# Performance work log

Hardware: AMD Instinct MI355X
Metric: run time of the kernel (lower is better)

Reference implementation:

```python
import jax, jax.numpy as jnp
import numpy as np

MODES1 = 20
MODES2 = 20
WIDTH = 64
NUM_LAYERS = 4
B, H, W = 8, 256, 256


def _conv2d(x, w, b, pad):
    # x: (B,C,H,W), w: (O,I,kh,kw)
    y = jax.lax.conv_general_dilated(
        x, w, window_strides=(1, 1), padding=[(pad, pad), (pad, pad)],
        dimension_numbers=('NCHW', 'OIHW', 'NCHW'))
    return y + b[None, :, None, None]


def _spectral_conv(x, w1, w2, m1, m2):
    # x: (B,C,H,W); w1,w2: (I,O,m1,m2,2) real/imag pairs
    h, w = x.shape[-2], x.shape[-1]
    x_ft = jnp.fft.rfft2(x, norm='ortho')              # (B,C,H,W//2+1) complex
    w1c = w1[..., 0] + 1j * w1[..., 1]
    w2c = w2[..., 0] + 1j * w2[..., 1]
    top = jnp.einsum('bixy,ioxy->boxy', x_ft[:, :, :m1, :m2], w1c)
    bot = jnp.einsum('bixy,ioxy->boxy', x_ft[:, :, -m1:, :m2], w2c)
    out_ft = jnp.zeros((x.shape[0], w1.shape[1], h, w // 2 + 1), dtype=x_ft.dtype)
    out_ft = out_ft.at[:, :, :m1, :m2].set(top)
    out_ft = out_ft.at[:, :, -m1:, :m2].set(bot)
    return jnp.fft.irfft2(out_ft, s=(h, w), norm='ortho')


def setup_inputs() -> dict:
    key = jax.random.key(0)
    ks = jax.random.split(key, 16)
    C = WIDTH
    L = NUM_LAYERS
    scale = 1.0 / (C * C)
    inp = {
        'x': jax.random.normal(ks[0], (B, H, W, 3), dtype=jnp.float32),
        'fc0_w': jax.random.normal(ks[1], (3, C), dtype=jnp.float32) * 0.1,
        'fc0_b': jnp.zeros((C,), dtype=jnp.float32),
        'w1': scale * jax.random.uniform(ks[2], (L, C, C, MODES1, MODES2, 2), dtype=jnp.float32),
        'w2': scale * jax.random.uniform(ks[3], (L, C, C, MODES1, MODES2, 2), dtype=jnp.float32),
        'convh_w': jax.random.normal(ks[4], (L, C, C, 3, 3), dtype=jnp.float32) * 0.02,
        'convh_b': jnp.zeros((L, C), dtype=jnp.float32),
        'convw_w': jax.random.normal(ks[5], (L, C, C, 3, 3), dtype=jnp.float32) * 0.02,
        'convw_b': jnp.zeros((L, C), dtype=jnp.float32),
        'pw_w': jax.random.normal(ks[6], (L, C, C, 1, 1), dtype=jnp.float32) * 0.05,
        'pw_b': jnp.zeros((L, C), dtype=jnp.float32),
        'fc1_w': jax.random.normal(ks[7], (C, 128), dtype=jnp.float32) * 0.05,
        'fc1_b': jnp.zeros((128,), dtype=jnp.float32),
        'fc2_w': jax.random.normal(ks[8], (128, 1), dtype=jnp.float32) * 0.05,
        'fc2_b': jnp.zeros((1,), dtype=jnp.float32),
    }
    return inp


def reference(x, fc0_w, fc0_b, w1, w2, convh_w, convh_b, convw_w, convw_b,
              pw_w, pw_b, fc1_w, fc1_b, fc2_w, fc2_b):
    # fc0 lift: (B,H,W,3) -> (B,H,W,C) -> (B,C,H,W)
    h = jnp.einsum('bhwc,cd->bhwd', x, fc0_w) + fc0_b
    h = jnp.transpose(h, (0, 3, 1, 2))
    for i in range(NUM_LAYERS):
        x1 = _spectral_conv(h, w1[i], w2[i], MODES1, MODES2)
        # Mamba fallback block: two 3x3 convs summed (LayerNorm unused in forward)
        x2 = _conv2d(h, convh_w[i], convh_b[i], 1) + _conv2d(h, convw_w[i], convw_b[i], 1)
        x3 = _conv2d(h, pw_w[i], pw_b[i], 0)
        h = x1 + x2 + x3
        if i < NUM_LAYERS - 1:
            h = jax.nn.gelu(h, approximate=False)
    h = jnp.transpose(h, (0, 2, 3, 1))                  # (B,H,W,C)
    h = jnp.einsum('bhwc,cd->bhwd', h, fc1_w) + fc1_b
    h = jax.nn.gelu(h, approximate=False)
    out = jnp.einsum('bhwc,cd->bhwd', h, fc2_w) + fc2_b  # (B,H,W,1)
    return out
```

## Files before the change

### kernel.cpp

```cpp
#include <hip/hip_runtime.h>
#include <math.h>

#define NB 8
#define NC 64
#define NH 256
#define NW 256
#define NM 40
#define NKX 20
#define NL 4

typedef _Float16 f16x8 __attribute__((ext_vector_type(8)));
typedef float    f32x4 __attribute__((ext_vector_type(4)));

#define PERCB_FLOATS ((size_t)(2*4194304 + 655360 + 2*102400))
#define FIXED_FLOATS ((size_t)(6553600 + 10240 + 20480 + 147456 + 256 + 167936 + 2048))

static __device__ __forceinline__ float gelu_f(float v) {
  return 0.5f * v * (1.f + erff(v * 0.70710678118654752f));
}
static __device__ __forceinline__ unsigned pack2(_Float16 a, _Float16 b) {
  union { _Float16 h[2]; unsigned u; } x; x.h[0] = a; x.h[1] = b; return x.u;
}

__global__ __launch_bounds__(256) void k_tables(float2* __restrict__ Tx,
                                                float2* __restrict__ Ty) {
  int t = blockIdx.x * 256 + threadIdx.x;
  const float w = (float)(2.0 * 3.14159265358979323846 / 256.0);
  if (t < NKX * 256) {
    int kx = t >> 8, x = t & 255;
    float th = (float)((kx * x) & 255) * w;
    Tx[t] = make_float2(cosf(th), sinf(th));
  }
  int u = t - NKX * 256;
  if (u >= 0 && u < NM * 256) {
    int m = u >> 8, y = u & 255;
    int ky = (m < 20) ? m : (m + 216);
    float th = (float)((ky * y) & 255) * w;
    Ty[u] = make_float2(cosf(th), sinf(th));
  }
}

__global__ __launch_bounds__(256) void k_txpack(_Float16* __restrict__ th,
                                                _Float16* __restrict__ tl) {
  int t = blockIdx.x * 256 + threadIdx.x;
  int j = t & 7, lane = (t >> 3) & 63;
  int rest = t >> 9;
  int nt = rest % 3, kc = rest / 3;
  int x = kc * 32 + ((lane >> 4) << 3) + j;
  int n = nt * 16 + (lane & 15);
  float val = 0.f;
  if (n < 40) {
    int kx = n >> 1;
    const float w = (float)(2.0 * 3.14159265358979323846 / 256.0);
    float ang = (float)((kx * x) & 255) * w;
    val = (n & 1) ? -sinf(ang) : cosf(ang);
  }
  _Float16 hi = (_Float16)val;
  th[t] = hi;
  tl[t] = (_Float16)(val - (float)hi);
}

__global__ __launch_bounds__(256) void k_wc(const float* __restrict__ ch,
                                            const float* __restrict__ cw,
                                            const float* __restrict__ pw,
                                            const float* __restrict__ chb,
                                            const float* __restrict__ cwb,
                                            const float* __restrict__ pwb,
                                            float* __restrict__ wc,
                                            float* __restrict__ bc) {
  int t = blockIdx.x * 256 + threadIdx.x;
  if (t < NL * NC * NC * 9) {
    int tap = t % 9;
    int io  = t / 9;
    int o   = io % 64;
    int i   = (io / 64) % 64;
    int l   = io / 4096;
    int src = ((l * 64 + o) * 64 + i) * 9 + tap;
    float v = ch[src] + cw[src];
    if (tap == 4) v += pw[(l * 64 + o) * 64 + i];
    wc[t] = v;
  }
  if (t < NL * NC) bc[t] = chb[t] + cwb[t] + pwb[t];
}

__global__ __launch_bounds__(256) void k_wpack(const float* __restrict__ wc,
                                               _Float16* __restrict__ whi,
                                               _Float16* __restrict__ wlo) {
  int t = blockIdx.x * 256 + threadIdx.x;
  int lane = t & 63;
  int nt   = (t >> 6) & 3;
  int chunk = (t >> 8) % 18;
  int l4   = t / 4608;
  int tap = chunk >> 1, half = chunk & 1;
  int o = nt * 16 + (lane & 15);
  _Float16 hi[8], lo[8];
  #pragma unroll
  for (int j = 0; j < 8; ++j) {
    int i = half * 32 + ((lane >> 4) << 3) + j;
    float v = wc[((l4 * 64 + i) * 64 + o) * 9 + tap];
    _Float16 h = (_Float16)v;
    hi[j] = h;
    lo[j] = (_Float16)(v - (float)h);
  }
  *(f16x8*)(whi + (size_t)t * 8) = *(f16x8*)hi;
  *(f16x8*)(wlo + (size_t)t * 8) = *(f16x8*)lo;
}

__global__ __launch_bounds__(256) void k_hpack(const float* __restrict__ w1,
                                               _Float16* __restrict__ whi,
                                               _Float16* __restrict__ wlo) {
  int t = blockIdx.x * 256 + threadIdx.x;
  int lane = t & 63;
  int nt   = (t >> 6) & 7;
  int chunk = t >> 9;
  int jo = nt * 16 + (lane & 15);
  _Float16 hi[8], lo[8];
  #pragma unroll
  for (int j = 0; j < 8; ++j) {
    int c = chunk * 32 + ((lane >> 4) << 3) + j;
    float v = w1[c * 128 + jo];
    _Float16 h = (_Float16)v;
    hi[j] = h;
    lo[j] = (_Float16)(v - (float)h);
  }
  *(f16x8*)(whi + (size_t)t * 8) = *(f16x8*)hi;
  *(f16x8*)(wlo + (size_t)t * 8) = *(f16x8*)lo;
}

__global__ __launch_bounds__(256) void k_fc0(const float* __restrict__ x,
                                             const float* __restrict__ w,
                                             const float* __restrict__ b,
                                             float* __restrict__ h, int b0) {
  int t = blockIdx.x * 256 + threadIdx.x;
  int ch = t & 63;
  int px = t >> 6;
  const float* xp = x + ((size_t)b0 * 65536 + px) * 3;
  h[t] = xp[0] * w[ch] + xp[1] * w[64 + ch] + xp[2] * w[128 + ch] + b[ch];
}

__global__ __launch_bounds__(256) void k_fwdx(const float* __restrict__ h,
                                              const f16x8* __restrict__ txh,
                                              const f16x8* __restrict__ txl,
                                              float2* __restrict__ Fx) {
  __shared__ _Float16 sH[64 * 136 * 2];
  int y = blockIdx.x & 255, bb = blockIdx.x >> 8;
  int tid = threadIdx.x;
  int w = tid >> 6, lane = tid & 63, quad = lane >> 4, l15 = lane & 15;
  const float* hp = h + ((size_t)(bb * 256 + y) * 256) * 64;

  f32x4 acc[3];
  #pragma unroll
  for (int nt = 0; nt < 3; ++nt) acc[nt] = (f32x4){0.f, 0.f, 0.f, 0.f};

  #pragma unroll 1
  for (int hs = 0; hs < 2; ++hs) {
    __syncthreads();
    #pragma unroll
    for (int it = 0; it < 8; ++it) {
      int e = it * 256 + tid;
      int xx = e >> 4;
      int chg = (e & 15) << 2;
      float4 v = *(const float4*)(hp + ((size_t)(hs * 128 + xx)) * 64 + chg);
      float vv[4] = {v.x, v.y, v.z, v.w};
      #pragma unroll
      for (int k = 0; k < 4; ++k) {
        _Float16 hi = (_Float16)vv[k];
        sH[(chg + k) * 136 + xx] = hi;
        sH[8704 + (chg + k) * 136 + xx] = (_Float16)(vv[k] - (float)hi);
      }
    }
    __syncthreads();
    #pragma unroll
    for (int kc = 0; kc < 4; ++kc) {
      int xb = kc * 32 + (quad << 3);
      f16x8 ah = *(const f16x8*)(sH + (w * 16 + l15) * 136 + xb);
      f16x8 al = *(const f16x8*)(sH + 8704 + (w * 16 + l15) * 136 + xb);
      int kcg = hs * 4 + kc;
      #pragma unroll
      for (int nt = 0; nt < 3; ++nt) {
        f16x8 bh = txh[(size_t)(kcg * 3 + nt) * 64 + lane];
        f16x8 bl = txl[(size_t)(kcg * 3 + nt) * 64 + lane];
        acc[nt] = __builtin_amdgcn_mfma_f32_16x16x32_f16(ah, bh, acc[nt], 0, 0, 0);
        acc[nt] = __builtin_amdgcn_mfma_f32_16x16x32_f16(ah, bl, acc[nt], 0, 0, 0);
        acc[nt] = __builtin_amdgcn_mfma_f32_16x16x32_f16(al, bh, acc[nt], 0, 0, 0);
      }
    }
  }
  #pragma unroll
  for (int nt = 0; nt < 3; ++nt) {
    int n = nt * 16 + l15;
    if (n < 40) {
      int kx = n >> 1, ri = n & 1;
      #pragma unroll
      for (int r = 0; r < 4; ++r) {
        int c = w * 16 + (quad << 2) + r;
        ((float*)(Fx + ((size_t)(bb * 64 + c) * 256 + y) * 20 + kx))[ri] = acc[nt][r];
      }
    }
  }
}

__global__ __launch_bounds__(256) void k_fwdy(const float2* __restrict__ Fx,
                                              const float2* __restrict__ Ty,
                                              float2* __restrict__ FxyT, int nbc) {
  __shared__ float2 sFx[5120];
  int bc = blockIdx.x;
  const float4* src = (const float4*)(Fx + (size_t)bc * 5120);
  float4* dst = (float4*)sFx;
  for (int e = threadIdx.x; e < 2560; e += 256) dst[e] = src[e];
  __syncthreads();
  for (int mk = threadIdx.x; mk < 800; mk += 256) {
    int kx = mk % 20, m = mk / 20;
    const float2* tp = Ty + m * 256;
    float re = 0.f, im = 0.f;
    #pragma unroll 4
    for (int yy = 0; yy < 256; ++yy) {
      float2 f = sFx[yy * 20 + kx];
      float2 wv = tp[yy];
      re += f.x * wv.x + f.y * wv.y;
      im += f.y * wv.x - f.x * wv.y;
    }
    FxyT[(size_t)mk * nbc + bc] = make_float2(re * (1.f / 256.f), im * (1.f / 256.f));
  }
}

__global__ __launch_bounds__(256) void k_wT(const float* __restrict__ w1,
                                            const float* __restrict__ w2,
                                            float2* __restrict__ wT, int l) {
  __shared__ float2 tile[32][33];
  int mk0 = blockIdx.x * 32;
  int io0 = blockIdx.y * 32;
  int tx = threadIdx.x & 31, ty0 = threadIdx.x >> 5;
  #pragma unroll
  for (int s = 0; s < 4; ++s) {
    int ty = ty0 * 4 + s;
    int mk = mk0 + tx, io = io0 + ty;
    int m = mk / 20, kx = mk % 20;
    const float* src = (m < 20) ? w1 : w2;
    int mm = (m < 20) ? m : (m - 20);
    size_t idx = ((((size_t)l * 4096 + io) * 20 + mm) * 20 + kx) * 2;
    tile[ty][tx] = make_float2(src[idx], src[idx + 1]);
  }
  __syncthreads();
  #pragma unroll
  for (int s = 0; s < 4; ++s) {
    int ty = ty0 * 4 + s;
    wT[(size_t)(mk0 + ty) * 4096 + (io0 + tx)] = tile[tx][ty];
  }
}

__global__ __launch_bounds__(256) void k_mix(const float2* __restrict__ FxyT,
                                             const float2* __restrict__ wT,
                                             float2* __restrict__ G, int nrows) {
  __shared__ float2 sf[512];
  int mk = blockIdx.x;
  for (int t = threadIdx.x; t < nrows; t += 256)
    sf[t] = FxyT[(size_t)mk * nrows + t];
  __syncthreads();
  const float2* wp = wT + (size_t)mk * 4096;
  for (int t = threadIdx.x; t < nrows; t += 256) {
    int b = t >> 6, o = t & 63;
    const float2* fb = sf + b * 64;
    float re = 0.f, im = 0.f;
    #pragma unroll 8
    for (int i = 0; i < 64; ++i) {
      float2 f = fb[i];
      float2 w = wp[i * 64 + o];
      re += f.x * w.x - f.y * w.y;
      im += f.x * w.y + f.y * w.x;
    }
    G[(size_t)(b * 64 + o) * 800 + mk] = make_float2(re, im);
  }
}

__global__ __launch_bounds__(256) void k_invy(const float2* __restrict__ G,
                                              const float2* __restrict__ Ty,
                                              float2* __restrict__ Gy) {
  int t  = blockIdx.x * 256 + threadIdx.x;
  int kx = t % 20;
  int y  = (t / 20) & 255;
  int bc = t / 5120;
  const float2* gp = G + (size_t)bc * 800 + kx;
  float re = 0.f, im = 0.f;
  #pragma unroll 4
  for (int m = 0; m < 40; ++m) {
    float2 g = gp[m * 20];
    float2 w = Ty[m * 256 + y];
    re += g.x * w.x - g.y * w.y;
    im += g.x * w.y + g.y * w.x;
  }
  Gy[t] = make_float2(re, im);
}

__global__ __launch_bounds__(256, 3) void k_conv(const float* __restrict__ hin,
                                                 const f16x8* __restrict__ wph,
                                                 const f16x8* __restrict__ wpl,
                                                 const float* __restrict__ bcb,
                                                 const float2* __restrict__ Gy,
                                                 const float2* __restrict__ Tx,
                                                 float* __restrict__ hout,
                                                 int dogelu, int bsh) {
  __shared__ unsigned sAu[13056];
  int bidx = blockIdx.x;
  int bb = bidx & ((1 << bsh) - 1);
  int rest = bidx >> bsh;
  int xt = rest & 7;
  int yt = (rest >> 3) & 63;
  int x0 = xt << 5, y0 = yt << 2;
  int tid = threadIdx.x;
  int w = tid >> 6, lane = tid & 63, quad = lane >> 4, l15 = lane & 15;

  float bias[4];
  #pragma unroll
  for (int nt = 0; nt < 4; ++nt) bias[nt] = bcb[nt * 16 + l15];

  for (int e = tid; e < 204 * 32; e += 256) {
    int px = e >> 5, chp = e & 31;
    int rg = px / 34, cg = px % 34;
    int gy = y0 - 1 + rg, gx = x0 - 1 + cg;
    float2 v = make_float2(0.f, 0.f);
    if (gy >= 0 && gy < 256 && gx >= 0 && gx < 256)
      v = *(const float2*)(hin + (((size_t)bb * 256 + gy) * 256 + gx) * 64 + chp * 2);
    _Float16 h0 = (_Float16)v.x, h1 = (_Float16)v.y;
    _Float16 l0 = (_Float16)(v.x - (float)h0), l1 = (_Float16)(v.y - (float)h1);
    int dw = (px << 5) + (chp ^ ((px & 7) << 2));
    sAu[dw] = pack2(h0, h1);
    sAu[6528 + dw] = pack2(l0, l1);
  }
  __syncthreads();

  f32x4 acc[2][4];
  #pragma unroll
  for (int s = 0; s < 2; ++s)
    #pragma unroll
    for (int nt = 0; nt < 4; ++nt) acc[s][nt] = (f32x4){0.f, 0.f, 0.f, 0.f};

  #pragma unroll 1
  for (int tap = 0; tap < 9; ++tap) {
    int dy = tap / 3, dx = tap % 3;
    #pragma unroll
    for (int half = 0; half < 2; ++half) {
      int chunk = tap * 2 + half;
      const f16x8* bh = wph + (size_t)(chunk * 4) * 64 + lane;
      const f16x8* bl = wpl + (size_t)(chunk * 4) * 64 + lane;
      f16x8 bfh[4], bfl[4];
      #pragma unroll
      for (int nt = 0; nt < 4; ++nt) { bfh[nt] = bh[nt * 64]; bfl[nt] = bl[nt * 64]; }
      f16x8 afh[2], afl[2];
      #pragma unroll
      for (int s = 0; s < 2; ++s) {
        int px = (w + dy) * 34 + (s * 16 + dx) + l15;
        int dw = (px << 5) + (((half << 4) + (quad << 2)) ^ ((px & 7) << 2));
        afh[s] = *(const f16x8*)(sAu + dw);
        afl[s] = *(const f16x8*)(sAu + 6528 + dw);
      }
      #pragma unroll
      for (int s = 0; s < 2; ++s)
        #pragma unroll
        for (int nt = 0; nt < 4; ++nt) {
          acc[s][nt] = __builtin_amdgcn_mfma_f32_16x16x32_f16(afh[s], bfh[nt], acc[s][nt], 0, 0, 0);
          acc[s][nt] = __builtin_amdgcn_mfma_f32_16x16x32_f16(afh[s], bfl[nt], acc[s][nt], 0, 0, 0);
          acc[s][nt] = __builtin_amdgcn_mfma_f32_16x16x32_f16(afl[s], bfh[nt], acc[s][nt], 0, 0, 0);
        }
    }
  }

  __syncthreads();
  float2* sT  = (float2*)sAu;
  float2* sGy = (float2*)(sAu + 1280);
  for (int e = tid; e < 640; e += 256) {
    int kx = e >> 5, col = e & 31;
    sT[e] = Tx[kx * 256 + x0 + col];
  }
  for (int e = tid; e < 5120; e += 256) {
    int o = e / 80, rem = e % 80;
    int row = rem / 20, kx = rem % 20;
    sGy[o * 82 + row * 20 + kx] =
        Gy[((size_t)(bb * 64 + o) * 256 + (y0 + row)) * 20 + kx];
  }
  __syncthreads();

  const float scale = 1.f / 256.f;
  #pragma unroll
  for (int s = 0; s < 2; ++s) {
    int colb = s * 16 + (quad << 2);
    #pragma unroll
    for (int nt = 0; nt < 4; ++nt) {
      int o = nt * 16 + l15;
      const float2* gp = sGy + o * 82 + w * 20;
      f32x4 sr = {0.f, 0.f, 0.f, 0.f};
      #pragma unroll
      for (int p = 0; p < 10; ++p) {
        float4 g = *(const float4*)(gp + 2 * p);
        float f0 = (p == 0) ? 1.f : 2.f;
        float4 tA = *(const float4*)(sT + (2 * p) * 32 + colb);
        float4 tB = *(const float4*)(sT + (2 * p) * 32 + colb + 2);
        sr.x += f0 * (g.x * tA.x - g.y * tA.y);
        sr.y += f0 * (g.x * tA.z - g.y * tA.w);
        sr.z += f0 * (g.x * tB.x - g.y * tB.y);
        sr.w += f0 * (g.x * tB.z - g.y * tB.w);
        float4 tC = *(const float4*)(sT + (2 * p + 1) * 32 + colb);
        float4 tD = *(const float4*)(sT + (2 * p + 1) * 32 + colb + 2);
        sr.x += 2.f * (g.z * tC.x - g.w * tC.y);
        sr.y += 2.f * (g.z * tC.z - g.w * tC.w);
        sr.z += 2.f * (g.z * tD.x - g.w * tD.y);
        sr.w += 2.f * (g.z * tD.z - g.w * tD.w);
      }
      #pragma unroll
      for (int r = 0; r < 4; ++r) {
        float v = acc[s][nt][r] + bias[nt] + sr[r] * scale;
        if (dogelu) v = gelu_f(v);
        acc[s][nt][r] = v;
      }
    }
  }

  __syncthreads();
  float* sF = (float*)sAu;
  #pragma unroll
  for (int s = 0; s < 2; ++s)
    #pragma unroll
    for (int nt = 0; nt < 4; ++nt)
      #pragma unroll
      for (int r = 0; r < 4; ++r) {
        int c = s * 16 + (quad << 2) + r;
        int seg = nt ^ ((c >> 2) & 3);
        sF[(w * 32 + c) * 64 + seg * 16 + l15] = acc[s][nt][r];
      }
  __syncthreads();

  float* op = hout + (((size_t)bb * 256 + (y0 + w)) * 256 + x0) * 64;
  #pragma unroll
  for (int i = 0; i < 8; ++i) {
    int chunk = i * 64 + lane;
    int c = chunk >> 4, ch4 = chunk & 15;
    int seg = (ch4 >> 2) ^ ((c >> 2) & 3);
    float4 v = *(const float4*)(sF + (w * 32 + c) * 64 + seg * 16 + (ch4 & 3) * 4);
    *(float4*)(op + c * 64 + ch4 * 4) = v;
  }
}

__global__ __launch_bounds__(256, 2) void k_head(const float* __restrict__ h,
                                                 const f16x8* __restrict__ whi,
                                                 const f16x8* __restrict__ wlo,
                                                 const float* __restrict__ b1,
                                                 const float* __restrict__ w2,
                                                 const float* __restrict__ b2,
                                                 float* __restrict__ out, int b0) {
  int tid = threadIdx.x;
  int w = tid >> 6, lane = tid & 63, quad = lane >> 4, l15 = lane & 15;
  int px0 = blockIdx.x * 64 + w * 16;

  f32x4 acc[8];
  #pragma unroll
  for (int nt = 0; nt < 8; ++nt) acc[nt] = (f32x4){0.f, 0.f, 0.f, 0.f};

  #pragma unroll
  for (int half = 0; half < 2; ++half) {
    const float* ap = h + (size_t)(px0 + l15) * 64 + half * 32 + quad * 8;
    float4 a0 = *(const float4*)ap;
    float4 a1 = *(const float4*)(ap + 4);
    _Float16 ah[8], al[8];
    float av[8] = {a0.x, a0.y, a0.z, a0.w, a1.x, a1.y, a1.z, a1.w};
    #pragma unroll
    for (int j = 0; j < 8; ++j) {
      ah[j] = (_Float16)av[j];
      al[j] = (_Float16)(av[j] - (float)ah[j]);
    }
    f16x8 afh = *(f16x8*)ah, afl = *(f16x8*)al;
    #pragma unroll
    for (int nt = 0; nt < 8; ++nt) {
      f16x8 bh = whi[(size_t)(half * 8 + nt) * 64 + lane];
      f16x8 bl = wlo[(size_t)(half * 8 + nt) * 64 + lane];
      acc[nt] = __builtin_amdgcn_mfma_f32_16x16x32_f16(afh, bh, acc[nt], 0, 0, 0);
      acc[nt] = __builtin_amdgcn_mfma_f32_16x16x32_f16(afh, bl, acc[nt], 0, 0, 0);
      acc[nt] = __builtin_amdgcn_mfma_f32_16x16x32_f16(afl, bh, acc[nt], 0, 0, 0);
    }
  }

  float part[4] = {0.f, 0.f, 0.f, 0.f};
  #pragma unroll
  for (int nt = 0; nt < 8; ++nt) {
    int jo = nt * 16 + l15;
    float bb1 = b1[jo], ww2 = w2[jo];
    #pragma unroll
    for (int r = 0; r < 4; ++r)
      part[r] += gelu_f(acc[nt][r] + bb1) * ww2;
  }
  #pragma unroll
  for (int r = 0; r < 4; ++r) {
    float v = part[r];
    v += __shfl_xor(v, 1);
    v += __shfl_xor(v, 2);
    v += __shfl_xor(v, 4);
    v += __shfl_xor(v, 8);
    if (l15 == 0)
      out[(size_t)b0 * 65536 + px0 + quad * 4 + r] = v + b2[0];
  }
}

extern "C" void kernel_launch(void* const* d_in, const int* in_sizes, int n_in,
                              void* d_out, int out_size, void* d_ws, size_t ws_size,
                              hipStream_t stream) {
  const float* x    = (const float*)d_in[0];
  const float* fc0w = (const float*)d_in[1];
  const float* fc0b = (const float*)d_in[2];
  const float* w1   = (const float*)d_in[3];
  const float* w2   = (const float*)d_in[4];
  const float* chw  = (const float*)d_in[5];
  const float* chb  = (const float*)d_in[6];
  const float* cww  = (const float*)d_in[7];
  const float* cwb  = (const float*)d_in[8];
  const float* pww  = (const float*)d_in[9];
  const float* pwb  = (const float*)d_in[10];
  const float* fc1w = (const float*)d_in[11];
  const float* fc1b = (const float*)d_in[12];
  const float* fc2w = (const float*)d_in[13];
  const float* fc2b = (const float*)d_in[14];

  int cb = 1;
  for (int cand = 8; cand >= 1; cand >>= 1) {
    size_t need = (PERCB_FLOATS * (size_t)cand + FIXED_FLOATS) * sizeof(float);
    if (ws_size >= need) { cb = cand; break; }
  }
  int bsh = (cb == 8) ? 3 : (cb == 4) ? 2 : (cb == 2) ? 1 : 0;

  const size_t szH = (size_t)cb * 4194304;

  float*  ws  = (float*)d_ws;
  float*  h   = ws;
  float*  h2  = h + szH;
  float2* Fx  = (float2*)(h2 + szH);
  float2* Fxy = (float2*)((float*)Fx + (size_t)cb * 655360);
  float2* G   = (float2*)((float*)Fxy + (size_t)cb * 102400);
  float2* wT  = (float2*)((float*)G + (size_t)cb * 102400);
  float2* Tx  = (float2*)((float*)wT + 6553600);
  float2* Ty  = (float2*)((float*)Tx + 10240);
  float*  wcb = (float*)Ty + 20480;
  float*  bcb = wcb + 147456;
  _Float16* wpkhi = (_Float16*)(bcb + 256);
  _Float16* wpklo = wpkhi + 147456;
  _Float16* w1hi  = wpklo + 147456;
  _Float16* w1lo  = w1hi + 8192;
  _Float16* txph  = w1lo + 8192;
  _Float16* txpl  = txph + 12288;
  float2* Gy = Fx;

  k_tables<<<60, 256, 0, stream>>>(Tx, Ty);
  k_txpack<<<48, 256, 0, stream>>>(txph, txpl);
  k_wc<<<576, 256, 0, stream>>>(chw, cww, pww, chb, cwb, pwb, wcb, bcb);
  k_wpack<<<72, 256, 0, stream>>>(wcb, wpkhi, wpklo);
  k_hpack<<<4, 256, 0, stream>>>(fc1w, w1hi, w1lo);

  for (int b0 = 0; b0 < NB; b0 += cb) {
    k_fc0<<<cb * 16384, 256, 0, stream>>>(x, fc0w, fc0b, h, b0);
    float* cur = h;
    float* nxt = h2;
    int nbc = cb * 64;
    for (int l = 0; l < NL; ++l) {
      k_fwdx<<<cb * 256, 256, 0, stream>>>(cur, (const f16x8*)txph,
                                           (const f16x8*)txpl, Fx);
      k_fwdy<<<nbc, 256, 0, stream>>>(Fx, Ty, Fxy, nbc);
      k_wT<<<dim3(25, 128), 256, 0, stream>>>(w1, w2, wT, l);
      k_mix<<<NM * NKX, 256, 0, stream>>>(Fxy, wT, G, nbc);
      k_invy<<<cb * 1280, 256, 0, stream>>>(G, Ty, Gy);
      k_conv<<<cb * 512, 256, 0, stream>>>(cur,
                                           (const f16x8*)(wpkhi + (size_t)l * 36864),
                                           (const f16x8*)(wpklo + (size_t)l * 36864),
                                           bcb + (size_t)l * 64, Gy, Tx, nxt,
                                           (l < NL - 1) ? 1 : 0, bsh);
      float* tmp = cur; cur = nxt; nxt = tmp;
    }
    k_head<<<cb * 1024, 256, 0, stream>>>(cur, (const f16x8*)w1hi, (const f16x8*)w1lo,
                                          fc1b, fc2w, fc2b, (float*)d_out, b0);
  }
}
```

Before: 4.394 ms.

## Fuse inverse y-DFT into conv kernel, dropping the separate k_invy pass

Removes the standalone k_invy kernel. Each conv block now computes the inverse y-transform for its own 4 rows directly from G and a shared-memory slice of Ty. This avoids writing and re-reading the Gy intermediate through global memory and saves a launch per layer. In exchange, each block recomputes 40x20 complex MACs per (o,row) with 40 live accumulators per thread, which may add register pressure at the launch bound of 3 blocks per CU. It also rereads G from global memory in every x-tile block.

```diff
diff --git a/kernel.cpp b/kernel.cpp
--- a/kernel.cpp
+++ b/kernel.cpp
@@ -273,30 +273,12 @@
   }
 }
 
-__global__ __launch_bounds__(256) void k_invy(const float2* __restrict__ G,
-                                              const float2* __restrict__ Ty,
-                                              float2* __restrict__ Gy) {
-  int t  = blockIdx.x * 256 + threadIdx.x;
-  int kx = t % 20;
-  int y  = (t / 20) & 255;
-  int bc = t / 5120;
-  const float2* gp = G + (size_t)bc * 800 + kx;
-  float re = 0.f, im = 0.f;
-  #pragma unroll 4
-  for (int m = 0; m < 40; ++m) {
-    float2 g = gp[m * 20];
-    float2 w = Ty[m * 256 + y];
-    re += g.x * w.x - g.y * w.y;
-    im += g.x * w.y + g.y * w.x;
-  }
-  Gy[t] = make_float2(re, im);
-}
-
 __global__ __launch_bounds__(256, 3) void k_conv(const float* __restrict__ hin,
                                                  const f16x8* __restrict__ wph,
                                                  const f16x8* __restrict__ wpl,
                                                  const float* __restrict__ bcb,
-                                                 const float2* __restrict__ Gy,
+                                                 const float2* __restrict__ G,
+                                                 const float2* __restrict__ Ty,
                                                  const float2* __restrict__ Tx,
                                                  float* __restrict__ hout,
                                                  int dogelu, int bsh) {
@@ -367,16 +349,42 @@
 
   __syncthreads();
   float2* sT  = (float2*)sAu;
-  float2* sGy = (float2*)(sAu + 1280);
+  float2* sTy = (float2*)sAu + 640;
+  float2* sGy = (float2*)sAu + 800;
   for (int e = tid; e < 640; e += 256) {
     int kx = e >> 5, col = e & 31;
     sT[e] = Tx[kx * 256 + x0 + col];
   }
-  for (int e = tid; e < 5120; e += 256) {
-    int o = e / 80, rem = e % 80;
-    int row = rem / 20, kx = rem % 20;
-    sGy[o * 82 + row * 20 + kx] =
-        Gy[((size_t)(bb * 64 + o) * 256 + (y0 + row)) * 20 + kx];
+  if (tid < 160) {
+    int m = tid >> 2, r = tid & 3;
+    sTy[tid] = Ty[m * 256 + y0 + r];
+  }
+  __syncthreads();
+
+  {
+    int o = tid >> 2, row = tid & 3;
+    const float2* gp = G + (size_t)(bb * 64 + o) * 800;
+    float re[20], im[20];
+    #pragma unroll
+    for (int kx = 0; kx < 20; ++kx) { re[kx] = 0.f; im[kx] = 0.f; }
+    #pragma unroll 2
+    for (int m = 0; m < 40; ++m) {
+      float2 t = sTy[m * 4 + row];
+      #pragma unroll
+      for (int p = 0; p < 10; ++p) {
+        float4 g = *(const float4*)(gp + m * 20 + 2 * p);
+        re[2 * p]     += g.x * t.x - g.y * t.y;
+        im[2 * p]     += g.x * t.y + g.y * t.x;
+        re[2 * p + 1] += g.z * t.x - g.w * t.y;
+        im[2 * p + 1] += g.z * t.y + g.w * t.x;
+      }
+    }
+    float2* dst = sGy + o * 82 + row * 20;
+    #pragma unroll
+    for (int p = 0; p < 10; ++p) {
+      float4 v = make_float4(re[2 * p], im[2 * p], re[2 * p + 1], im[2 * p + 1]);
+      *(float4*)(dst + 2 * p) = v;
+    }
   }
   __syncthreads();
 
@@ -544,7 +552,6 @@
   _Float16* w1lo  = w1hi + 8192;
   _Float16* txph  = w1lo + 8192;
   _Float16* txpl  = txph + 12288;
-  float2* Gy = Fx;
 
   k_tables<<<60, 256, 0, stream>>>(Tx, Ty);
   k_txpack<<<48, 256, 0, stream>>>(txph, txpl);
@@ -563,11 +570,10 @@
       k_fwdy<<<nbc, 256, 0, stream>>>(Fx, Ty, Fxy, nbc);
       k_wT<<<dim3(25, 128), 256, 0, stream>>>(w1, w2, wT, l);
       k_mix<<<NM * NKX, 256, 0, stream>>>(Fxy, wT, G, nbc);
-      k_invy<<<cb * 1280, 256, 0, stream>>>(G, Ty, Gy);
       k_conv<<<cb * 512, 256, 0, stream>>>(cur,
                                            (const f16x8*)(wpkhi + (size_t)l * 36864),
                                            (const f16x8*)(wpklo + (size_t)l * 36864),
-                                           bcb + (size_t)l * 64, Gy, Tx, nxt,
+                                           bcb + (size_t)l * 64, G, Ty, Tx, nxt,
                                            (l < NL - 1) ? 1 : 0, bsh);
       float* tmp = cur; cur = nxt; nxt = tmp;
     }
```

Result: slower. 4.565 ms (+3.9%).
